# Optimization experiments

Measured on AMD Instinct MI355X. Metric: run time of the kernel, lower is better.

Reference implementation:

```python
import jax, jax.numpy as jnp
import numpy as np

BETA = 0.9
THR = 1.0
ALPHA = 2.0  # snntorch ATan surrogate default

@jax.custom_vjp
def spike(x):
    # Heaviside spike with ATan surrogate gradient (snntorch default)
    return (x > 0).astype(x.dtype)

def _spike_fwd(x):
    return spike(x), x

def _spike_bwd(x, g):
    grad = (ALPHA / 2.0) / (1.0 + (jnp.pi / 2.0 * ALPHA * x) ** 2)
    return (g * grad,)

spike.defvjp(_spike_fwd, _spike_bwd)

def setup_inputs() -> dict:
    key = jax.random.key(0)
    k1, k2, k3 = jax.random.split(key, 3)
    T, B, NI, NH, NO = 250, 256, 700, 1024, 20
    input_spikes = (jax.random.uniform(k1, (T, B, NI)) < 0.1).astype(jnp.float32)
    W1 = jax.random.normal(k2, (NH, NI), dtype=jnp.float32) / np.float32(np.sqrt(NI))
    W2 = jax.random.normal(k3, (NO, NH), dtype=jnp.float32) / np.float32(np.sqrt(NH))
    return {"input_spikes": input_spikes, "W1": W1, "W2": W2}

def reference(input_spikes, W1, W2):
    # fc1 over all timesteps in one GEMM: [T,B,NI] x [NH,NI] -> [T,B,NH]
    cur1 = jnp.einsum('tbi,hi->tbh', input_spikes, W1)

    # snntorch Leaky (reset_mechanism='subtract'):
    #   reset = detach(heaviside(mem_prev - thr))
    #   mem   = beta*mem_prev + cur - reset*thr
    #   spk   = heaviside(mem - thr)
    def lif_step(mem, c):
        reset = jax.lax.stop_gradient(spike(mem - THR))
        mem = BETA * mem + c - reset * THR
        spk = spike(mem - THR)
        return mem, spk

    mem0 = jnp.zeros(cur1.shape[1:], cur1.dtype)
    _, spk1 = jax.lax.scan(lif_step, mem0, cur1)  # [T,B,NH]

    # fc2 over all timesteps: [T,B,NH] x [NO,NH] -> [T,B,NO]
    cur2 = jnp.einsum('tbh,oh->tbo', spk1, W2)

    # Readout: Leaky with reset_mechanism='none' -> mem = beta*mem + cur
    def ro_step(mem, c):
        mem = BETA * mem + c
        return mem, mem

    m0 = jnp.zeros(cur2.shape[1:], cur2.dtype)
    _, mem_out_rec = jax.lax.scan(ro_step, m0, cur2)  # [T,B,NO]

    out_rec = jax.nn.softmax(mem_out_rec, axis=2)  # torch softmax dim=1 on [B,NO]
    return mem_out_rec, out_rec
```

## Files before the change

kernel.cpp:

```cpp
#include <hip/hip_runtime.h>
#include <hip/hip_bf16.h>
#include <cstdint>

#define T_STEPS 250
#define BATCH   256
#define NI      700
#define NH      1024
#define NO      20
#define BETAF   0.9f
#define KPAD    704
#define KT_N    22
#define KCAT    2112

typedef __attribute__((ext_vector_type(8))) short bf16x8;
typedef __attribute__((ext_vector_type(4))) float f32x4;

static __device__ __forceinline__ unsigned short f2bu(float x) {
    union { __hip_bfloat16 h; unsigned short u; } c;
    c.h = __float2bfloat16(x);
    return c.u;
}
static __device__ __forceinline__ float b2f(unsigned short u) {
    union { __hip_bfloat16 h; unsigned short u; } c;
    c.u = u;
    return __bfloat162float(c.h);
}

__global__ __launch_bounds__(256) void k0_init(const float* __restrict__ W1,
                                               const float* __restrict__ W2,
                                               float* __restrict__ W2T,
                                               float* __restrict__ mem1,
                                               unsigned short* __restrict__ Bcat) {
    int idx = blockIdx.x * 256 + threadIdx.x;
    if (idx < BATCH * NH) mem1[idx] = 0.f;
    if (idx < NH * NO) {
        int h = idx / NO, o = idx % NO;
        W2T[idx] = W2[o * NH + h];
    }
    if (idx < NH * KPAD) {
        int n = idx / KPAD, k = idx % KPAD;
        float w = (k < NI) ? W1[n * NI + k] : 0.f;
        unsigned short hu = f2bu(w);
        float r1 = w - b2f(hu);
        unsigned short mu = f2bu(r1);
        float r2 = r1 - b2f(mu);
        unsigned short lu = f2bu(r2);
        unsigned short* row = Bcat + (size_t)n * KCAT + k;
        row[0]        = hu;
        row[KPAD]     = mu;
        row[2 * KPAD] = lu;
    }
}

__global__ __launch_bounds__(256) void k1_cvt(const float* __restrict__ A,
                                              unsigned short* __restrict__ Abf,
                                              int rows) {
    int idx = blockIdx.x * 256 + threadIdx.x;
    int r = idx / 176, q = idx - r * 176;
    if (r >= rows) return;
    int k = q * 4;
    ushort4 o = make_ushort4(0, 0, 0, 0);
    if (k < NI) {
        float4 v = *(const float4*)(A + (size_t)r * NI + k);
        o.x = f2bu(v.x); o.y = f2bu(v.y); o.z = f2bu(v.z); o.w = f2bu(v.w);
    }
    *(ushort4*)(Abf + (size_t)r * KPAD + k) = o;
}

__global__ __launch_bounds__(256) void k2_fc1(const unsigned short* __restrict__ Abf,
                                              const unsigned short* __restrict__ Bcat,
                                              float* __restrict__ C) {
    __shared__ unsigned short As[128 * 32];
    __shared__ unsigned short Bs[3][128 * 32];
    const int tid  = threadIdx.x;
    const int lane = tid & 63;
    const int wv   = tid >> 6;

    int nwg = gridDim.x, bid = blockIdx.x, w;
    if ((nwg & 7) == 0) w = (bid & 7) * (nwg >> 3) + (bid >> 3);
    else                w = bid;
    const int brow = (w >> 3) * 128;
    const int bn   = (w & 7) * 128;
    const int wm   = (wv >> 1) * 64;
    const int wn   = (wv & 1) * 64;

    f32x4 acc[4][4];
#pragma unroll
    for (int i = 0; i < 4; ++i)
#pragma unroll
        for (int j = 0; j < 4; ++j) acc[i][j] = (f32x4){0.f, 0.f, 0.f, 0.f};

    auto stage = [&](const unsigned short* gbase, int rstride, int kcol,
                     unsigned short* lds) {
#pragma unroll
        for (int j = 0; j < 2; ++j) {
            int c   = wv * 128 + j * 64 + lane;
            int row = c >> 2;
            int lk  = ((c & 3) ^ ((row >> 1) & 3)) * 8;
            const unsigned short* src = gbase + (size_t)row * rstride + kcol + lk;
            __builtin_amdgcn_global_load_lds(
                (const __attribute__((address_space(1))) void*)src,
                (__attribute__((address_space(3))) void*)(lds + (wv * 128 + j * 64) * 8),
                16, 0, 0);
        }
    };

    const unsigned short* Ab = Abf + (size_t)brow * KPAD;
    const unsigned short* Bb = Bcat + (size_t)bn * KCAT;

    const int frow = lane & 15;
    const int fsl  = (((lane >> 4) & 3) ^ ((frow >> 1) & 3)) * 8;

    for (int kt = 0; kt < KT_N; ++kt) {
        stage(Ab, KPAD, kt * 32, As);
#pragma unroll
        for (int s = 0; s < 3; ++s)
            stage(Bb, KCAT, s * KPAD + kt * 32, Bs[s]);
        __syncthreads();

        bf16x8 a[4];
#pragma unroll
        for (int i = 0; i < 4; ++i)
            a[i] = *(const bf16x8*)&As[(wm + i * 16 + frow) * 32 + fsl];
#pragma unroll
        for (int s = 0; s < 3; ++s) {
#pragma unroll
            for (int j = 0; j < 4; ++j) {
                bf16x8 b = *(const bf16x8*)&Bs[s][(wn + j * 16 + frow) * 32 + fsl];
#pragma unroll
                for (int i = 0; i < 4; ++i)
                    acc[i][j] = __builtin_amdgcn_mfma_f32_16x16x32_bf16(a[i], b, acc[i][j], 0, 0, 0);
            }
        }
        __syncthreads();
    }

#pragma unroll
    for (int i = 0; i < 4; ++i) {
#pragma unroll
        for (int j = 0; j < 4; ++j) {
            int col  = bn + wn + j * 16 + (lane & 15);
            int row0 = brow + wm + i * 16 + ((lane >> 4) << 2);
#pragma unroll
            for (int q = 0; q < 4; ++q)
                C[(size_t)(row0 + q) * NH + col] = acc[i][j][q];
        }
    }
}

__global__ __launch_bounds__(256) void k3_lif(const float* __restrict__ cur1,
                                              float* __restrict__ mem1,
                                              unsigned long long* __restrict__ bits,
                                              int TC) {
    int b = blockIdx.x >> 2;
    int hg = blockIdx.x & 3;
    int h = hg * 256 + threadIdx.x;
    const size_t S = (size_t)BATCH * NH;
    const float* p = cur1 + (size_t)b * NH + h;
    unsigned long long* bp = bits + (size_t)b * 16 + hg * 4 + (threadIdx.x >> 6);
    const bool lead = (threadIdx.x & 63) == 0;
    float mem = mem1[b * NH + h];

#define LIF_STEP(cv, t)                                                        \
    {                                                                          \
        float reset = (mem > 1.0f) ? 1.0f : 0.0f;                              \
        mem = fmaf(BETAF, mem, (cv)) - reset;                                  \
        unsigned long long mk = __ballot(mem > 1.0f);                          \
        if (lead) bp[(size_t)(t) * (BATCH * 16)] = mk;                         \
    }

    float c0 = (0 < TC) ? p[0] : 0.f;
    float c1 = (1 < TC) ? p[S] : 0.f;
    float c2 = (2 < TC) ? p[2 * S] : 0.f;
    float c3 = (3 < TC) ? p[3 * S] : 0.f;
    int tc = 0;
    for (; tc + 4 <= TC; tc += 4) {
        LIF_STEP(c0, tc + 0); if (tc + 4 < TC) c0 = p[(size_t)(tc + 4) * S];
        LIF_STEP(c1, tc + 1); if (tc + 5 < TC) c1 = p[(size_t)(tc + 5) * S];
        LIF_STEP(c2, tc + 2); if (tc + 6 < TC) c2 = p[(size_t)(tc + 6) * S];
        LIF_STEP(c3, tc + 3); if (tc + 7 < TC) c3 = p[(size_t)(tc + 7) * S];
    }
    for (; tc < TC; ++tc) { float c = p[(size_t)tc * S]; LIF_STEP(c, tc); }
#undef LIF_STEP
    mem1[b * NH + h] = mem;
}

__global__ __launch_bounds__(256) void k4_fc2(const unsigned long long* __restrict__ bits,
                                              const float* __restrict__ W2T,
                                              float* __restrict__ cur2) {
    __shared__ float part[4][NO];
    int row  = blockIdx.x;
    int wv   = threadIdx.x >> 6;
    int lane = threadIdx.x & 63;
    bool act = lane < NO;
    unsigned long long mv = (lane < 4) ? bits[(size_t)row * 16 + wv * 4 + lane] : 0ULL;
    const float* W = W2T + (act ? lane : 0);
    float p0 = 0.f, p1 = 0.f;
#pragma unroll
    for (int i = 0; i < 4; ++i) {
        unsigned long long m = __shfl(mv, i);
        int base = (wv * 4 + i) * 64;
        while (m) {
            int  b0 = __ffsll(m) - 1;            m &= m - 1;
            bool v1 = m != 0;
            int  b1 = v1 ? __ffsll(m) - 1 : 0;   m &= m - 1;
            float w0 = W[(base + b0) * NO];
            float w1 = W[(base + b1) * NO];
            p0 += w0;
            p1 += v1 ? w1 : 0.f;
        }
    }
    float p = p0 + p1;
    if (wv != 0 && act) part[wv][lane] = p;
    __syncthreads();
    if (wv == 0 && act) {
        p += part[1][lane] + part[2][lane] + part[3][lane];
        cur2[(size_t)row * NO + lane] = p;
    }
}

__global__ __launch_bounds__(256) void k5_readout(const float* __restrict__ cur2,
                                                  float* __restrict__ out_mem,
                                                  float* __restrict__ out_sm) {
    int b = blockIdx.x * 8 + (threadIdx.x >> 5);
    int o = threadIdx.x & 31;
    bool act = o < NO;
    const float* p = cur2 + (size_t)b * NO + (act ? o : 0);
    float mem = 0.f;
    float nxt = p[0];
    for (int t = 0; t < T_STEPS; ++t) {
        float c = nxt;
        if (t + 1 < T_STEPS) nxt = p[(size_t)(t + 1) * BATCH * NO];
        mem = fmaf(BETAF, mem, c);
        float e = act ? __expf(mem) : 0.f;
        float s = e;
#pragma unroll
        for (int off = 16; off; off >>= 1) s += __shfl_xor(s, off, 32);
        if (act) {
            int base = (t * BATCH + b) * NO;
            out_mem[base + o] = mem;
            out_sm[base + o] = __fdividef(e, s);
        }
    }
}

extern "C" void kernel_launch(void* const* d_in, const int* in_sizes, int n_in,
                              void* d_out, int out_size, void* d_ws, size_t ws_size,
                              hipStream_t stream) {
    const float* spikes = (const float*)d_in[0];
    const float* W1     = (const float*)d_in[1];
    const float* W2     = (const float*)d_in[2];
    float* out_mem = (float*)d_out;
    float* out_sm  = out_mem + (size_t)T_STEPS * BATCH * NO;

    char* ws = (char*)d_ws;
    size_t off = 0;
    auto alloc = [&](size_t bytes) -> char* {
        off = (off + 255) & ~(size_t)255;
        char* p = ws + off;
        off += bytes;
        return p;
    };
    float*          W2T  = (float*)alloc((size_t)NH * NO * 4);
    float*          mem1 = (float*)alloc((size_t)BATCH * NH * 4);
    float*          cur2 = (float*)alloc((size_t)T_STEPS * BATCH * NO * 4);
    unsigned short* Bcat = (unsigned short*)alloc((size_t)NH * KCAT * 2);

    size_t fixed = (off + 255) & ~(size_t)255;
    size_t rem = ws_size > fixed ? ws_size - fixed : 0;
    size_t per_t = (size_t)BATCH * NH * 4 + (size_t)BATCH * KPAD * 2
                 + (size_t)BATCH * 16 * 8 + 768;
    int TC = (int)(rem / per_t);
    if (TC > T_STEPS) TC = T_STEPS;
    if (TC < 1) TC = 1;
    float*              cur1 = (float*)alloc((size_t)TC * BATCH * NH * 4);
    unsigned short*     Abf  = (unsigned short*)alloc((size_t)TC * BATCH * KPAD * 2);
    unsigned long long* bits = (unsigned long long*)alloc((size_t)TC * BATCH * 16 * 8);

    k0_init<<<(NH * KPAD + 255) / 256, 256, 0, stream>>>(W1, W2, W2T, mem1, Bcat);

    for (int t0 = 0; t0 < T_STEPS; t0 += TC) {
        int tc = T_STEPS - t0 < TC ? T_STEPS - t0 : TC;
        int rows = tc * BATCH;
        k1_cvt<<<(rows * 176 + 255) / 256, 256, 0, stream>>>(
            spikes + (size_t)t0 * BATCH * NI, Abf, rows);
        int nwg = (rows / 128) * 8;
        k2_fc1<<<nwg, 256, 0, stream>>>(Abf, Bcat, cur1);
        k3_lif<<<1024, 256, 0, stream>>>(cur1, mem1, bits, tc);
        k4_fc2<<<rows, 256, 0, stream>>>(bits, W2T, cur2 + (size_t)t0 * BATCH * NO);
    }

    k5_readout<<<32, 256, 0, stream>>>(cur2, out_mem, out_sm);
}
```

Baseline: 533.3 us.

## Vectorize LIF over neuron pairs, one wave per fc2 row, spread readout

Each LIF thread now handles two adjacent hidden neurons with float2 loads and writes two ballot masks at once, which halves the block count and changes the spike-bit layout to interleaved even/odd neurons. The fc2 kernel is adjusted to decode the new bit layout, and each wave now owns a whole row, so the shared-memory reduction and __syncthreads are gone. The readout kernel uses 64-thread blocks across 128 blocks to spread the serial time loop over more CUs. Tail loads in LIF are clamped instead of branched, so some redundant loads happen at the end of a chunk.

```diff
diff --git a/kernel.cpp b/kernel.cpp
--- a/kernel.cpp
+++ b/kernel.cpp
@@ -152,77 +152,82 @@
                                               float* __restrict__ mem1,
                                               unsigned long long* __restrict__ bits,
                                               int TC) {
-    int b = blockIdx.x >> 2;
-    int hg = blockIdx.x & 3;
-    int h = hg * 256 + threadIdx.x;
+    const int b    = blockIdx.x >> 1;
+    const int half = blockIdx.x & 1;
+    const int wv   = threadIdx.x >> 6;
+    const int lane = threadIdx.x & 63;
+    const int h    = half * 512 + wv * 128 + lane * 2;
     const size_t S = (size_t)BATCH * NH;
     const float* p = cur1 + (size_t)b * NH + h;
-    unsigned long long* bp = bits + (size_t)b * 16 + hg * 4 + (threadIdx.x >> 6);
-    const bool lead = (threadIdx.x & 63) == 0;
-    float mem = mem1[b * NH + h];
-
-#define LIF_STEP(cv, t)                                                        \
+    unsigned long long* bp = bits + (size_t)b * 16 + (half * 4 + wv) * 2;
+    const bool lead = lane == 0;
+
+    float2 mm = *(const float2*)(mem1 + b * NH + h);
+    float m0 = mm.x, m1 = mm.y;
+
+    auto ld = [&](int t) -> float2 {
+        int tt = t < TC ? t : TC - 1;
+        return *(const float2*)(p + (size_t)tt * S);
+    };
+
+#define K3_STEP(cv, t)                                                         \
     {                                                                          \
-        float reset = (mem > 1.0f) ? 1.0f : 0.0f;                              \
-        mem = fmaf(BETAF, mem, (cv)) - reset;                                  \
-        unsigned long long mk = __ballot(mem > 1.0f);                          \
-        if (lead) bp[(size_t)(t) * (BATCH * 16)] = mk;                         \
-    }
-
-    float c0 = (0 < TC) ? p[0] : 0.f;
-    float c1 = (1 < TC) ? p[S] : 0.f;
-    float c2 = (2 < TC) ? p[2 * S] : 0.f;
-    float c3 = (3 < TC) ? p[3 * S] : 0.f;
+        float r0 = (m0 > 1.f) ? 1.f : 0.f;                                     \
+        m0 = fmaf(BETAF, m0, (cv).x) - r0;                                     \
+        float r1 = (m1 > 1.f) ? 1.f : 0.f;                                     \
+        m1 = fmaf(BETAF, m1, (cv).y) - r1;                                     \
+        unsigned long long w0 = __ballot(m0 > 1.f);                            \
+        unsigned long long w1 = __ballot(m1 > 1.f);                            \
+        if (lead) {                                                            \
+            ulonglong2 v; v.x = w0; v.y = w1;                                  \
+            *(ulonglong2*)(bp + (size_t)(t) * (BATCH * 16)) = v;               \
+        }                                                                      \
+    }
+
+    float2 c0 = ld(0), c1 = ld(1), c2 = ld(2), c3 = ld(3);
     int tc = 0;
     for (; tc + 4 <= TC; tc += 4) {
-        LIF_STEP(c0, tc + 0); if (tc + 4 < TC) c0 = p[(size_t)(tc + 4) * S];
-        LIF_STEP(c1, tc + 1); if (tc + 5 < TC) c1 = p[(size_t)(tc + 5) * S];
-        LIF_STEP(c2, tc + 2); if (tc + 6 < TC) c2 = p[(size_t)(tc + 6) * S];
-        LIF_STEP(c3, tc + 3); if (tc + 7 < TC) c3 = p[(size_t)(tc + 7) * S];
-    }
-    for (; tc < TC; ++tc) { float c = p[(size_t)tc * S]; LIF_STEP(c, tc); }
-#undef LIF_STEP
-    mem1[b * NH + h] = mem;
+        K3_STEP(c0, tc + 0); c0 = ld(tc + 4);
+        K3_STEP(c1, tc + 1); c1 = ld(tc + 5);
+        K3_STEP(c2, tc + 2); c2 = ld(tc + 6);
+        K3_STEP(c3, tc + 3); c3 = ld(tc + 7);
+    }
+    for (; tc < TC; ++tc) { float2 c = ld(tc); K3_STEP(c, tc); }
+#undef K3_STEP
+    float2 mo; mo.x = m0; mo.y = m1;
+    *(float2*)(mem1 + b * NH + h) = mo;
 }
 
 __global__ __launch_bounds__(256) void k4_fc2(const unsigned long long* __restrict__ bits,
                                               const float* __restrict__ W2T,
                                               float* __restrict__ cur2) {
-    __shared__ float part[4][NO];
-    int row  = blockIdx.x;
-    int wv   = threadIdx.x >> 6;
+    int row  = blockIdx.x * 4 + (threadIdx.x >> 6);
     int lane = threadIdx.x & 63;
     bool act = lane < NO;
-    unsigned long long mv = (lane < 4) ? bits[(size_t)row * 16 + wv * 4 + lane] : 0ULL;
+    unsigned long long mv = (lane < 16) ? bits[(size_t)row * 16 + lane] : 0ULL;
     const float* W = W2T + (act ? lane : 0);
     float p0 = 0.f, p1 = 0.f;
 #pragma unroll
-    for (int i = 0; i < 4; ++i) {
+    for (int i = 0; i < 16; ++i) {
         unsigned long long m = __shfl(mv, i);
-        int base = (wv * 4 + i) * 64;
+        int base = (i >> 1) * 128 + (i & 1);
         while (m) {
             int  b0 = __ffsll(m) - 1;            m &= m - 1;
             bool v1 = m != 0;
             int  b1 = v1 ? __ffsll(m) - 1 : 0;   m &= m - 1;
-            float w0 = W[(base + b0) * NO];
-            float w1 = W[(base + b1) * NO];
+            float w0 = W[(base + 2 * b0) * NO];
+            float w1 = W[(base + 2 * b1) * NO];
             p0 += w0;
             p1 += v1 ? w1 : 0.f;
         }
     }
-    float p = p0 + p1;
-    if (wv != 0 && act) part[wv][lane] = p;
-    __syncthreads();
-    if (wv == 0 && act) {
-        p += part[1][lane] + part[2][lane] + part[3][lane];
-        cur2[(size_t)row * NO + lane] = p;
-    }
-}
-
-__global__ __launch_bounds__(256) void k5_readout(const float* __restrict__ cur2,
-                                                  float* __restrict__ out_mem,
-                                                  float* __restrict__ out_sm) {
-    int b = blockIdx.x * 8 + (threadIdx.x >> 5);
+    if (act) cur2[(size_t)row * NO + lane] = p0 + p1;
+}
+
+__global__ __launch_bounds__(64) void k5_readout(const float* __restrict__ cur2,
+                                                 float* __restrict__ out_mem,
+                                                 float* __restrict__ out_sm) {
+    int b = blockIdx.x * 2 + (threadIdx.x >> 5);
     int o = threadIdx.x & 31;
     bool act = o < NO;
     const float* p = cur2 + (size_t)b * NO + (act ? o : 0);
@@ -286,9 +291,9 @@
             spikes + (size_t)t0 * BATCH * NI, Abf, rows);
         int nwg = (rows / 128) * 8;
         k2_fc1<<<nwg, 256, 0, stream>>>(Abf, Bcat, cur1);
-        k3_lif<<<1024, 256, 0, stream>>>(cur1, mem1, bits, tc);
-        k4_fc2<<<rows, 256, 0, stream>>>(bits, W2T, cur2 + (size_t)t0 * BATCH * NO);
-    }
-
-    k5_readout<<<32, 256, 0, stream>>>(cur2, out_mem, out_sm);
-}
+        k3_lif<<<512, 256, 0, stream>>>(cur1, mem1, bits, tc);
+        k4_fc2<<<rows / 4, 256, 0, stream>>>(bits, W2T, cur2 + (size_t)t0 * BATCH * NO);
+    }
+
+    k5_readout<<<128, 64, 0, stream>>>(cur2, out_mem, out_sm);
+}
```

Result: faster. 521.0 us (-2.3%).
